# Kernel tuning notes

Measured on AMD Instinct MI355X. Metric: run time of the kernel, lower is better.

Reference implementation:

```python
import jax, jax.numpy as jnp
import numpy as np

B, C, H, W = 8, 256, 64, 64
CQK = C // 8  # 32


def setup_inputs() -> dict:
    key = jax.random.key(0)
    ks = jax.random.split(key, 8)
    s = 0.05
    return {
        "x": jax.random.normal(ks[0], (B, C, H, W), dtype=jnp.float32),
        "wq": jax.random.normal(ks[1], (CQK, C), dtype=jnp.float32) * s,
        "bq": jax.random.normal(ks[2], (CQK,), dtype=jnp.float32) * s,
        "wk": jax.random.normal(ks[3], (CQK, C), dtype=jnp.float32) * s,
        "bk": jax.random.normal(ks[4], (CQK,), dtype=jnp.float32) * s,
        "wv": jax.random.normal(ks[5], (C, C), dtype=jnp.float32) * s,
        "bv": jax.random.normal(ks[6], (C,), dtype=jnp.float32) * s,
        "gamma": jax.random.normal(ks[7], (1,), dtype=jnp.float32),
    }


def reference(x, wq, bq, wk, bk, wv, bv, gamma):
    b, c, h, w = x.shape
    xf = x.reshape(b, c, h * w)  # [B, C, N]
    # conv1d kernel-size-1 == per-token linear over channels
    f = jnp.einsum('oc,bcn->bon', wq, xf) + bq[None, :, None]  # [B, C/8, N]
    g = jnp.einsum('oc,bcn->bon', wk, xf) + bk[None, :, None]  # [B, C/8, N]
    hh = jnp.einsum('oc,bcn->bon', wv, xf) + bv[None, :, None]  # [B, C, N]
    # scores[b, i, j] = sum_o f[b, o, i] * g[b, o, j]; NO 1/sqrt(d) scaling
    scores = jnp.einsum('boi,boj->bij', f, g)  # [B, N, N]
    # softmax over dim=1 (the f/query index axis), as in the original
    beta = jax.nn.softmax(scores, axis=1)
    # o[b, c, j] = gamma * sum_i hh[b, c, i] * beta[b, i, j] + xf
    o = gamma[0] * jnp.einsum('bci,bij->bcj', hh, beta) + xf
    return o.reshape(b, c, h, w)
```

## Files before the change

### kernel.cpp

```cpp
#include <hip/hip_runtime.h>
#include <stdint.h>

#define B_ 8
#define C_ 256
#define N_ 4096
#define LOG2E 1.44269504088896f
#define NSHIFT_L2E (-14.0f * 1.44269504088896f)

typedef _Float16 half8 __attribute__((ext_vector_type(8)));
typedef _Float16 half4 __attribute__((ext_vector_type(4)));
typedef __fp16  fp16x2 __attribute__((ext_vector_type(2)));
typedef float floatx4 __attribute__((ext_vector_type(4)));

__global__ __launch_bounds__(256) void k_wprep(const float* __restrict__ wq, const float* __restrict__ bq,
                                               const float* __restrict__ wk, const float* __restrict__ bk,
                                               const float* __restrict__ wv, const float* __restrict__ bv,
                                               _Float16* __restrict__ Whf, float* __restrict__ Bh) {
    int r = blockIdx.x;
    int t = threadIdx.x;
    const float* src;
    float bias;
    if (r < 32)      { src = wq + r * 256;        bias = bq[r]; }
    else if (r < 64) { src = wk + (r - 32) * 256; bias = bk[r - 32]; }
    else             { src = wv + (r - 64) * 256; bias = bv[r - 64]; }
    Whf[(t >> 3) * 2560 + r * 8 + (t & 7)] = (_Float16)src[t];
    if (t == 0) Bh[r] = bias;
}

__global__ __launch_bounds__(256) void k_proj(const float* __restrict__ x,
                                              const _Float16* __restrict__ Whf,
                                              const float* __restrict__ Bh,
                                              _Float16* __restrict__ Kf,
                                              _Float16* __restrict__ Qf,
                                              _Float16* __restrict__ Vf) {
    __shared__ float xtile[64 * 65];
    __shared__ _Float16 As[64 * 264] __attribute__((aligned(16)));
    int id = blockIdx.x;
    int b  = id & 7;
    int i0 = (id >> 3) * 64;
    int t = threadIdx.x;
    int w = t >> 6, lane = t & 63, col = lane & 15, q = lane >> 4;
    const float* xb = x + (size_t)b * C_ * N_ + i0;
    for (int cc = 0; cc < 4; ++cc) {
        int cr = t >> 4;
        int ip = (t & 15) * 4;
#pragma unroll
        for (int k = 0; k < 4; ++k)
            *(float4*)&xtile[(cr + 16 * k) * 65 + ip] =
                *(const float4*)&xb[(size_t)(cc * 64 + cr + 16 * k) * N_ + ip];
        __syncthreads();
        int i = t & 63, cb2 = (t >> 6) * 16;
        float v[16];
#pragma unroll
        for (int k = 0; k < 16; ++k) v[k] = xtile[(cb2 + k) * 65 + i];
        half8 h0, h1;
#pragma unroll
        for (int k = 0; k < 8; ++k) { h0[k] = (_Float16)v[k]; h1[k] = (_Float16)v[8 + k]; }
        *(half8*)&As[i * 264 + cc * 64 + cb2] = h0;
        *(half8*)&As[i * 264 + cc * 64 + cb2 + 8] = h1;
        __syncthreads();
    }
    floatx4 acc[4][5];
#pragma unroll
    for (int mt = 0; mt < 4; ++mt)
#pragma unroll
        for (int nt = 0; nt < 5; ++nt) acc[mt][nt] = (floatx4){0.f, 0.f, 0.f, 0.f};
    for (int kc = 0; kc < 8; ++kc) {
        half8 a[4], bf[5];
#pragma unroll
        for (int nt = 0; nt < 5; ++nt)
            bf[nt] = *(const half8*)&Whf[(kc * 4 + q) * 2560 + (w * 80 + nt * 16 + col) * 8];
#pragma unroll
        for (int mt = 0; mt < 4; ++mt)
            a[mt] = *(const half8*)&As[(mt * 16 + col) * 264 + kc * 32 + q * 8];
#pragma unroll
        for (int mt = 0; mt < 4; ++mt)
#pragma unroll
            for (int nt = 0; nt < 5; ++nt)
                acc[mt][nt] = __builtin_amdgcn_mfma_f32_16x16x32_f16(a[mt], bf[nt], acc[mt][nt], 0, 0, 0);
    }
#pragma unroll
    for (int nt = 0; nt < 5; ++nt) {
        int n = w * 80 + nt * 16 + col;
        float bias = Bh[n];
        if (n < 32) {
#pragma unroll
            for (int mt = 0; mt < 4; ++mt)
#pragma unroll
                for (int r = 0; r < 4; ++r) {
                    int i = i0 + mt * 16 + q * 4 + r;
                    Kf[((((size_t)b * 128 + (i >> 5)) * 4 + (n >> 3)) * 32 + (i & 31)) * 8 + (n & 7)]
                        = (_Float16)((acc[mt][nt][r] + bias) * LOG2E);
                }
        } else if (n < 64) {
            int n2 = n - 32;
#pragma unroll
            for (int mt = 0; mt < 4; ++mt)
#pragma unroll
                for (int r = 0; r < 4; ++r) {
                    int j = i0 + mt * 16 + q * 4 + r;
                    Qf[((((size_t)b * 128 + (j >> 5)) * 4 + (n2 >> 3)) * 32 + (j & 31)) * 8 + (n2 & 7)]
                        = (_Float16)(acc[mt][nt][r] + bias);
                }
        } else {
            int c = n - 64;
#pragma unroll
            for (int mt = 0; mt < 4; ++mt) {
                int ib = (i0 >> 4) + mt;
                half4 v4;
#pragma unroll
                for (int r = 0; r < 4; ++r) v4[r] = (_Float16)(acc[mt][nt][r] + bias);
                *(half4*)&Vf[(((size_t)b * 256 + ib) * 256 + c) * 16 + q * 4] = v4;
            }
        }
    }
}

#define PS_BUF 4096

#define ATTN_STEP(IT, VCUR, VNXT, ROFF, WOFF)                                     \
    {                                                                             \
        if ((IT) < 63) {                                                          \
            _Pragma("unroll")                                                     \
            for (int ct = 0; ct < 2; ++ct) {                                      \
                VNXT[ct * 2 + 0] = *(const half8*)(pV0 + ct * 256);               \
                VNXT[ct * 2 + 1] = *(const half8*)(pV1 + ct * 256);               \
            }                                                                     \
            pV0 += 16384; pV1 += 16384;                                           \
            aKn0 = *(const half8*)(pK);                                           \
            aKn1 = *(const half8*)(pK + 128);                                     \
            pK += 2048;                                                           \
        }                                                                         \
        _Pragma("unroll")                                                         \
        for (int kk = 0; kk < 2; ++kk) {                                          \
            half8 bfr[4];                                                         \
            _Pragma("unroll")                                                     \
            for (int jt = 0; jt < 4; ++jt)                                        \
                bfr[jt] = *(const half8*)&PsF[(ROFF) + jt * 1024 + (kk ? ro1 : ro0)]; \
            _Pragma("unroll")                                                     \
            for (int ct = 0; ct < 2; ++ct)                                        \
                _Pragma("unroll")                                                 \
                for (int jt = 0; jt < 4; ++jt)                                    \
                    acc[ct][jt] = __builtin_amdgcn_mfma_f32_16x16x32_f16(         \
                        VCUR[ct * 2 + kk], bfr[jt], acc[ct][jt], 0, 0, 0);        \
        }                                                                         \
        if ((IT) < 63) {                                                          \
            _Pragma("unroll")                                                     \
            for (int itl = 0; itl < 2; ++itl) {                                   \
                floatx4 s = __builtin_amdgcn_mfma_f32_16x16x32_f16(               \
                    itl ? aKn1 : aKn0, bq, cns, 0, 0, 0);                         \
                float p0 = exp2f(s[0]);                                           \
                float p1 = exp2f(s[1]);                                           \
                float p2 = exp2f(s[2]);                                           \
                float p3 = exp2f(s[3]);                                           \
                lacc += (p0 + p1) + (p2 + p3);                                    \
                union { fp16x2 v; uint32_t u; } plo, phi;                         \
                plo.v = __builtin_amdgcn_cvt_pkrtz(p0, p1);                       \
                phi.v = __builtin_amdgcn_cvt_pkrtz(p2, p3);                       \
                uint2 pw; pw.x = plo.u; pw.y = phi.u;                             \
                *(uint2*)&PsF[(WOFF) + (itl ? wo1 : wo0)] = pw;                   \
            }                                                                     \
        }                                                                         \
        asm volatile("s_waitcnt lgkmcnt(0)\n\ts_barrier" ::: "memory");           \
    }

__global__ __launch_bounds__(512, 4) void k_attn(const _Float16* __restrict__ Kf,
                                                 const _Float16* __restrict__ Qf,
                                                 const _Float16* __restrict__ Vf,
                                                 const float* __restrict__ x,
                                                 const float* __restrict__ gptr,
                                                 float* __restrict__ out) {
    __shared__ _Float16 PsF[2 * PS_BUF] __attribute__((aligned(16)));
    __shared__ float Lp[2][64];
    int id = blockIdx.x;
    int b  = id & 7;
    int j0 = (id >> 3) * 64;
    int t = threadIdx.x;
    int w = t >> 6, lane = t & 63, col = lane & 15, q = lane >> 4;
    int jts = w & 3, ihs = w >> 2;
    int cw  = w * 32;
    const _Float16* Kfb = Kf + (size_t)b * 131072;
    const _Float16* Qfb = Qf + (size_t)b * 131072;
    const _Float16* Vfb = Vf + (size_t)b * 1048576;
    const _Float16* pK  = Kfb + ((ihs * 4 + q) * 32 + col) * 8;
    const _Float16* pV0 = Vfb + ((q >> 1) * 256 + cw + col) * 16 + (q & 1) * 8;
    const _Float16* pV1 = pV0 + 8192;
    const int cswz = col & 7;
    const int ro0 = col * 64 + ((q ^ cswz) << 3);
    const int ro1 = ro0 ^ 32;
    const int wo0 = (jts * 16 + col) * 64 + (((ihs << 2) ^ (q >> 1) ^ cswz) << 3) + (q & 1) * 4;
    const int wo1 = wo0 ^ 16;
    const floatx4 cns = {NSHIFT_L2E, NSHIFT_L2E, NSHIFT_L2E, NSHIFT_L2E};
    floatx4 acc[2][4];
#pragma unroll
    for (int ct = 0; ct < 2; ++ct)
#pragma unroll
        for (int jt = 0; jt < 4; ++jt) acc[ct][jt] = (floatx4){0.f, 0.f, 0.f, 0.f};
    float lacc = 0.f;
    half8 vA[4], vB[4], aKn0, aKn1;
#pragma unroll
    for (int ct = 0; ct < 2; ++ct) {
        vA[ct * 2 + 0] = *(const half8*)(pV0 + ct * 256);
        vA[ct * 2 + 1] = *(const half8*)(pV1 + ct * 256);
    }
    pV0 += 16384; pV1 += 16384;
    aKn0 = *(const half8*)(pK);
    aKn1 = *(const half8*)(pK + 128);
    pK += 2048;
    int jj = j0 + jts * 16;
    half8 bq = *(const half8*)&Qfb[(((jj >> 5) * 4 + q) * 32 + ((jj & 31) + col)) * 8];
#pragma unroll
    for (int itl = 0; itl < 2; ++itl) {
        floatx4 s = __builtin_amdgcn_mfma_f32_16x16x32_f16(itl ? aKn1 : aKn0, bq, cns, 0, 0, 0);
        float p0 = exp2f(s[0]);
        float p1 = exp2f(s[1]);
        float p2 = exp2f(s[2]);
        float p3 = exp2f(s[3]);
        lacc += (p0 + p1) + (p2 + p3);
        union { fp16x2 v; uint32_t u; } plo, phi;
        plo.v = __builtin_amdgcn_cvt_pkrtz(p0, p1);
        phi.v = __builtin_amdgcn_cvt_pkrtz(p2, p3);
        uint2 pw; pw.x = plo.u; pw.y = phi.u;
        *(uint2*)&PsF[itl ? wo1 : wo0] = pw;
    }
    asm volatile("s_waitcnt lgkmcnt(0)\n\ts_barrier" ::: "memory");
    for (int m = 0; m < 32; ++m) {
        int it = m * 2;
        ATTN_STEP(it,     vA, vB, 0,      PS_BUF)
        ATTN_STEP(it + 1, vB, vA, PS_BUF, 0)
    }
    lacc += __shfl_xor(lacc, 16, 64);
    lacc += __shfl_xor(lacc, 32, 64);
    if (lane < 16) Lp[ihs][jts * 16 + lane] = lacc;
    __syncthreads();
    float gamma = gptr[0];
    const float* xb = x + (size_t)b * C_ * N_;
    float* ob = out + (size_t)b * C_ * N_;
#pragma unroll
    for (int jt = 0; jt < 4; ++jt) {
        int jl = jt * 16 + col;
        float li = 1.0f / (Lp[0][jl] + Lp[1][jl]);
        int j = j0 + jl;
#pragma unroll
        for (int ct = 0; ct < 2; ++ct)
#pragma unroll
            for (int r = 0; r < 4; ++r) {
                int c = cw + ct * 16 + q * 4 + r;
                size_t off = (size_t)c * N_ + j;
                ob[off] = gamma * acc[ct][jt][r] * li + xb[off];
            }
    }
}

extern "C" void kernel_launch(void* const* d_in, const int* in_sizes, int n_in,
                              void* d_out, int out_size, void* d_ws, size_t ws_size,
                              hipStream_t stream) {
    const float* x  = (const float*)d_in[0];
    const float* wq = (const float*)d_in[1];
    const float* bq = (const float*)d_in[2];
    const float* wk = (const float*)d_in[3];
    const float* bk = (const float*)d_in[4];
    const float* wv = (const float*)d_in[5];
    const float* bv = (const float*)d_in[6];
    const float* gm = (const float*)d_in[7];
    float* out = (float*)d_out;
    char* ws = (char*)d_ws;
    _Float16* Vf  = (_Float16*)ws;
    _Float16* Kf  = (_Float16*)(ws + 16777216);
    _Float16* Qf  = (_Float16*)(ws + 18874368);
    _Float16* Whf = (_Float16*)(ws + 20971520);
    float*    Bh  = (float*)(ws + 21135360);

    k_wprep<<<dim3(320), 256, 0, stream>>>(wq, bq, wk, bk, wv, bv, Whf, Bh);
    k_proj<<<dim3(512), 256, 0, stream>>>(x, Whf, Bh, Kf, Qf, Vf);
    k_attn<<<dim3(512), 512, 0, stream>>>(Kf, Qf, Vf, x, gm, out);
}
```

Measured before the change: 190.2 us.

## Enlarge attention tile to 128 query columns per block, halving block count

Each attention block now covers 128 output columns instead of 64, so each V tile loaded from global memory serves twice as many columns and total V traffic is halved. Each wave now owns 64 channels and 64 columns (a 4x4 accumulator tile) and computes all four key sub-blocks for its own 16 columns, which removes the cross-wave partial row-sum combine. The shared P buffer doubles, and register use per thread rises (more accumulators and V fragments), so occupancy drops to 2 blocks per CU and the grid is 256 blocks.

```diff
diff --git a/kernel.cpp b/kernel.cpp
--- a/kernel.cpp
+++ b/kernel.cpp
@@ -116,19 +116,36 @@
     }
 }
 
-#define PS_BUF 4096
+#define PS_HALF 8192
+
+#define ATTN_SBLK(T, AK, WOFF)                                                    \
+    {                                                                             \
+        floatx4 s = __builtin_amdgcn_mfma_f32_16x16x32_f16(AK, bq, cns, 0, 0, 0); \
+        float p0 = exp2f(s[0]);                                                   \
+        float p1 = exp2f(s[1]);                                                   \
+        float p2 = exp2f(s[2]);                                                   \
+        float p3 = exp2f(s[3]);                                                   \
+        lacc += (p0 + p1) + (p2 + p3);                                            \
+        union { fp16x2 v; uint32_t u; } plo, phi;                                 \
+        plo.v = __builtin_amdgcn_cvt_pkrtz(p0, p1);                               \
+        phi.v = __builtin_amdgcn_cvt_pkrtz(p2, p3);                               \
+        uint2 pw; pw.x = plo.u; pw.y = phi.u;                                     \
+        *(uint2*)&PsF[(WOFF) + wo##T] = pw;                                       \
+    }
 
 #define ATTN_STEP(IT, VCUR, VNXT, ROFF, WOFF)                                     \
     {                                                                             \
         if ((IT) < 63) {                                                          \
             _Pragma("unroll")                                                     \
-            for (int ct = 0; ct < 2; ++ct) {                                      \
+            for (int ct = 0; ct < 4; ++ct) {                                      \
                 VNXT[ct * 2 + 0] = *(const half8*)(pV0 + ct * 256);               \
                 VNXT[ct * 2 + 1] = *(const half8*)(pV1 + ct * 256);               \
             }                                                                     \
             pV0 += 16384; pV1 += 16384;                                           \
-            aKn0 = *(const half8*)(pK);                                           \
-            aKn1 = *(const half8*)(pK + 128);                                     \
+            aK0 = *(const half8*)(pK);                                            \
+            aK1 = *(const half8*)(pK + 128);                                      \
+            aK2 = *(const half8*)(pK + 1024);                                     \
+            aK3 = *(const half8*)(pK + 1152);                                     \
             pK += 2048;                                                           \
         }                                                                         \
         _Pragma("unroll")                                                         \
@@ -138,114 +155,96 @@
             for (int jt = 0; jt < 4; ++jt)                                        \
                 bfr[jt] = *(const half8*)&PsF[(ROFF) + jt * 1024 + (kk ? ro1 : ro0)]; \
             _Pragma("unroll")                                                     \
-            for (int ct = 0; ct < 2; ++ct)                                        \
+            for (int ct = 0; ct < 4; ++ct)                                        \
                 _Pragma("unroll")                                                 \
                 for (int jt = 0; jt < 4; ++jt)                                    \
                     acc[ct][jt] = __builtin_amdgcn_mfma_f32_16x16x32_f16(         \
                         VCUR[ct * 2 + kk], bfr[jt], acc[ct][jt], 0, 0, 0);        \
         }                                                                         \
         if ((IT) < 63) {                                                          \
-            _Pragma("unroll")                                                     \
-            for (int itl = 0; itl < 2; ++itl) {                                   \
-                floatx4 s = __builtin_amdgcn_mfma_f32_16x16x32_f16(               \
-                    itl ? aKn1 : aKn0, bq, cns, 0, 0, 0);                         \
-                float p0 = exp2f(s[0]);                                           \
-                float p1 = exp2f(s[1]);                                           \
-                float p2 = exp2f(s[2]);                                           \
-                float p3 = exp2f(s[3]);                                           \
-                lacc += (p0 + p1) + (p2 + p3);                                    \
-                union { fp16x2 v; uint32_t u; } plo, phi;                         \
-                plo.v = __builtin_amdgcn_cvt_pkrtz(p0, p1);                       \
-                phi.v = __builtin_amdgcn_cvt_pkrtz(p2, p3);                       \
-                uint2 pw; pw.x = plo.u; pw.y = phi.u;                             \
-                *(uint2*)&PsF[(WOFF) + (itl ? wo1 : wo0)] = pw;                   \
-            }                                                                     \
+            ATTN_SBLK(0, aK0, WOFF)                                               \
+            ATTN_SBLK(1, aK1, WOFF)                                               \
+            ATTN_SBLK(2, aK2, WOFF)                                               \
+            ATTN_SBLK(3, aK3, WOFF)                                               \
         }                                                                         \
         asm volatile("s_waitcnt lgkmcnt(0)\n\ts_barrier" ::: "memory");           \
     }
 
-__global__ __launch_bounds__(512, 4) void k_attn(const _Float16* __restrict__ Kf,
+__global__ __launch_bounds__(512, 2) void k_attn(const _Float16* __restrict__ Kf,
                                                  const _Float16* __restrict__ Qf,
                                                  const _Float16* __restrict__ Vf,
                                                  const float* __restrict__ x,
                                                  const float* __restrict__ gptr,
                                                  float* __restrict__ out) {
-    __shared__ _Float16 PsF[2 * PS_BUF] __attribute__((aligned(16)));
-    __shared__ float Lp[2][64];
+    __shared__ _Float16 PsF[2 * PS_HALF] __attribute__((aligned(16)));
+    __shared__ float Lp[128];
     int id = blockIdx.x;
     int b  = id & 7;
-    int j0 = (id >> 3) * 64;
+    int j0 = (id >> 3) * 128;
     int t = threadIdx.x;
     int w = t >> 6, lane = t & 63, col = lane & 15, q = lane >> 4;
-    int jts = w & 3, ihs = w >> 2;
-    int cw  = w * 32;
+    int cs = w & 3, jh = w >> 2;
     const _Float16* Kfb = Kf + (size_t)b * 131072;
     const _Float16* Qfb = Qf + (size_t)b * 131072;
     const _Float16* Vfb = Vf + (size_t)b * 1048576;
-    const _Float16* pK  = Kfb + ((ihs * 4 + q) * 32 + col) * 8;
-    const _Float16* pV0 = Vfb + ((q >> 1) * 256 + cw + col) * 16 + (q & 1) * 8;
+    const _Float16* pK  = Kfb + q * 256 + col * 8;
+    const _Float16* pV0 = Vfb + ((q >> 1) * 256 + cs * 64 + col) * 16 + (q & 1) * 8;
     const _Float16* pV1 = pV0 + 8192;
     const int cswz = col & 7;
-    const int ro0 = col * 64 + ((q ^ cswz) << 3);
+    const int ro0 = (jh * 64 + col) * 64 + ((q ^ cswz) << 3);
     const int ro1 = ro0 ^ 32;
-    const int wo0 = (jts * 16 + col) * 64 + (((ihs << 2) ^ (q >> 1) ^ cswz) << 3) + (q & 1) * 4;
-    const int wo1 = wo0 ^ 16;
+    const int wo0 = (w * 16 + col) * 64 + (((0 + (q >> 1)) ^ cswz) << 3) + (q & 1) * 4;
+    const int wo1 = (w * 16 + col) * 64 + (((2 + (q >> 1)) ^ cswz) << 3) + (q & 1) * 4;
+    const int wo2 = (w * 16 + col) * 64 + (((4 + (q >> 1)) ^ cswz) << 3) + (q & 1) * 4;
+    const int wo3 = (w * 16 + col) * 64 + (((6 + (q >> 1)) ^ cswz) << 3) + (q & 1) * 4;
     const floatx4 cns = {NSHIFT_L2E, NSHIFT_L2E, NSHIFT_L2E, NSHIFT_L2E};
-    floatx4 acc[2][4];
-#pragma unroll
-    for (int ct = 0; ct < 2; ++ct)
+    floatx4 acc[4][4];
+#pragma unroll
+    for (int ct = 0; ct < 4; ++ct)
 #pragma unroll
         for (int jt = 0; jt < 4; ++jt) acc[ct][jt] = (floatx4){0.f, 0.f, 0.f, 0.f};
     float lacc = 0.f;
-    half8 vA[4], vB[4], aKn0, aKn1;
-#pragma unroll
-    for (int ct = 0; ct < 2; ++ct) {
+    half8 vA[8], vB[8], aK0, aK1, aK2, aK3;
+#pragma unroll
+    for (int ct = 0; ct < 4; ++ct) {
         vA[ct * 2 + 0] = *(const half8*)(pV0 + ct * 256);
         vA[ct * 2 + 1] = *(const half8*)(pV1 + ct * 256);
     }
     pV0 += 16384; pV1 += 16384;
-    aKn0 = *(const half8*)(pK);
-    aKn1 = *(const half8*)(pK + 128);
+    aK0 = *(const half8*)(pK);
+    aK1 = *(const half8*)(pK + 128);
+    aK2 = *(const half8*)(pK + 1024);
+    aK3 = *(const half8*)(pK + 1152);
     pK += 2048;
-    int jj = j0 + jts * 16;
-    half8 bq = *(const half8*)&Qfb[(((jj >> 5) * 4 + q) * 32 + ((jj & 31) + col)) * 8];
-#pragma unroll
-    for (int itl = 0; itl < 2; ++itl) {
-        floatx4 s = __builtin_amdgcn_mfma_f32_16x16x32_f16(itl ? aKn1 : aKn0, bq, cns, 0, 0, 0);
-        float p0 = exp2f(s[0]);
-        float p1 = exp2f(s[1]);
-        float p2 = exp2f(s[2]);
-        float p3 = exp2f(s[3]);
-        lacc += (p0 + p1) + (p2 + p3);
-        union { fp16x2 v; uint32_t u; } plo, phi;
-        plo.v = __builtin_amdgcn_cvt_pkrtz(p0, p1);
-        phi.v = __builtin_amdgcn_cvt_pkrtz(p2, p3);
-        uint2 pw; pw.x = plo.u; pw.y = phi.u;
-        *(uint2*)&PsF[itl ? wo1 : wo0] = pw;
-    }
+    int jj = j0 + w * 16;
+    half8 bq = *(const half8*)&Qfb[(((jj >> 5) * 4 + q) * 256 + ((jj & 31) + col) * 8)];
+    ATTN_SBLK(0, aK0, 0)
+    ATTN_SBLK(1, aK1, 0)
+    ATTN_SBLK(2, aK2, 0)
+    ATTN_SBLK(3, aK3, 0)
     asm volatile("s_waitcnt lgkmcnt(0)\n\ts_barrier" ::: "memory");
     for (int m = 0; m < 32; ++m) {
         int it = m * 2;
-        ATTN_STEP(it,     vA, vB, 0,      PS_BUF)
-        ATTN_STEP(it + 1, vB, vA, PS_BUF, 0)
+        ATTN_STEP(it,     vA, vB, 0,       PS_HALF)
+        ATTN_STEP(it + 1, vB, vA, PS_HALF, 0)
     }
     lacc += __shfl_xor(lacc, 16, 64);
     lacc += __shfl_xor(lacc, 32, 64);
-    if (lane < 16) Lp[ihs][jts * 16 + lane] = lacc;
+    if (lane < 16) Lp[w * 16 + lane] = lacc;
     __syncthreads();
     float gamma = gptr[0];
     const float* xb = x + (size_t)b * C_ * N_;
     float* ob = out + (size_t)b * C_ * N_;
 #pragma unroll
     for (int jt = 0; jt < 4; ++jt) {
-        int jl = jt * 16 + col;
-        float li = 1.0f / (Lp[0][jl] + Lp[1][jl]);
+        int jl = jh * 64 + jt * 16 + col;
+        float li = 1.0f / Lp[jl];
         int j = j0 + jl;
 #pragma unroll
-        for (int ct = 0; ct < 2; ++ct)
+        for (int ct = 0; ct < 4; ++ct)
 #pragma unroll
             for (int r = 0; r < 4; ++r) {
-                int c = cw + ct * 16 + q * 4 + r;
+                int c = cs * 64 + ct * 16 + q * 4 + r;
                 size_t off = (size_t)c * N_ + j;
                 ob[off] = gamma * acc[ct][jt][r] * li + xb[off];
             }
@@ -273,5 +272,5 @@
 
     k_wprep<<<dim3(320), 256, 0, stream>>>(wq, bq, wk, bk, wv, bv, Whf, Bh);
     k_proj<<<dim3(512), 256, 0, stream>>>(x, Whf, Bh, Kf, Qf, Vf);
-    k_attn<<<dim3(512), 512, 0, stream>>>(Kf, Qf, Vf, x, gm, out);
-}
+    k_attn<<<dim3(256), 512, 0, stream>>>(Kf, Qf, Vf, x, gm, out);
+}
```

Result: slower. 208.4 us (+9.6%).

## Double the i-block per barrier and raise MFMA wave priority

Applied to the files above, without the earlier changes.

Each barrier-separated step of the attention loop now covers two 64-row i-blocks: the P staging buffer doubles to 8192 halves per buffer, the loop runs 16 iterations of paired steps instead of 32, and the shared-memory swizzle offsets are rewritten for the wider row stride. This halves the number of workgroup barriers and lets score computation for two sub-blocks interleave with the PV MFMAs. s_setprio is raised around the PV MFMA block so waves issuing matrix work get scheduling priority. The cost is more LDS per block (32 KB vs 16 KB), which may lower occupancy at 4 blocks per CU, and more complex indexing.

```diff
diff --git a/kernel.cpp b/kernel.cpp
--- a/kernel.cpp
+++ b/kernel.cpp
@@ -116,51 +116,65 @@
     }
 }
 
-#define PS_BUF 4096
-
-#define ATTN_STEP(IT, VCUR, VNXT, ROFF, WOFF)                                     \
+#define PS_BUF 8192
+
+#define ATTN_SBLK(AK, WO)                                                         \
     {                                                                             \
-        if ((IT) < 63) {                                                          \
+        floatx4 s = __builtin_amdgcn_mfma_f32_16x16x32_f16(AK, bq, cns, 0, 0, 0); \
+        float p0 = exp2f(s[0]);                                                   \
+        float p1 = exp2f(s[1]);                                                   \
+        float p2 = exp2f(s[2]);                                                   \
+        float p3 = exp2f(s[3]);                                                   \
+        lacc += (p0 + p1) + (p2 + p3);                                            \
+        union { fp16x2 v; uint32_t u; } plo, phi;                                 \
+        plo.v = __builtin_amdgcn_cvt_pkrtz(p0, p1);                               \
+        phi.v = __builtin_amdgcn_cvt_pkrtz(p2, p3);                               \
+        uint2 pw; pw.x = plo.u; pw.y = phi.u;                                     \
+        *(uint2*)&PsF[WO] = pw;                                                   \
+    }
+
+#define ATTN_SUB(COND, H, VC, VN, KKA, KKB, ROFF, WOFF)                           \
+    {                                                                             \
+        if (COND) {                                                               \
+            aK0 = *(const half8*)(pK);                                            \
+            aK1 = *(const half8*)(pK + 128);                                      \
+            pK += 2048;                                                           \
+        }                                                                         \
+        if ((H) == 0 || (COND)) {                                                 \
             _Pragma("unroll")                                                     \
             for (int ct = 0; ct < 2; ++ct) {                                      \
-                VNXT[ct * 2 + 0] = *(const half8*)(pV0 + ct * 256);               \
-                VNXT[ct * 2 + 1] = *(const half8*)(pV1 + ct * 256);               \
+                VN[ct * 2 + 0] = *(const half8*)(pV0 + ct * 256);                 \
+                VN[ct * 2 + 1] = *(const half8*)(pV1 + ct * 256);                 \
             }                                                                     \
             pV0 += 16384; pV1 += 16384;                                           \
-            aKn0 = *(const half8*)(pK);                                           \
-            aKn1 = *(const half8*)(pK + 128);                                     \
-            pK += 2048;                                                           \
-        }                                                                         \
+        }                                                                         \
+        __builtin_amdgcn_s_setprio(1);                                            \
         _Pragma("unroll")                                                         \
         for (int kk = 0; kk < 2; ++kk) {                                          \
             half8 bfr[4];                                                         \
             _Pragma("unroll")                                                     \
             for (int jt = 0; jt < 4; ++jt)                                        \
-                bfr[jt] = *(const half8*)&PsF[(ROFF) + jt * 1024 + (kk ? ro1 : ro0)]; \
+                bfr[jt] = *(const half8*)&PsF[(ROFF) + jt * 2048 +                \
+                    ((kk ? (KKB) : (KKA)) & 1 ? ro1 : ro0) +                      \
+                    ((kk ? (KKB) : (KKA)) >> 1) * 64];                            \
             _Pragma("unroll")                                                     \
             for (int ct = 0; ct < 2; ++ct)                                        \
                 _Pragma("unroll")                                                 \
                 for (int jt = 0; jt < 4; ++jt)                                    \
                     acc[ct][jt] = __builtin_amdgcn_mfma_f32_16x16x32_f16(         \
-                        VCUR[ct * 2 + kk], bfr[jt], acc[ct][jt], 0, 0, 0);        \
-        }                                                                         \
-        if ((IT) < 63) {                                                          \
-            _Pragma("unroll")                                                     \
-            for (int itl = 0; itl < 2; ++itl) {                                   \
-                floatx4 s = __builtin_amdgcn_mfma_f32_16x16x32_f16(               \
-                    itl ? aKn1 : aKn0, bq, cns, 0, 0, 0);                         \
-                float p0 = exp2f(s[0]);                                           \
-                float p1 = exp2f(s[1]);                                           \
-                float p2 = exp2f(s[2]);                                           \
-                float p3 = exp2f(s[3]);                                           \
-                lacc += (p0 + p1) + (p2 + p3);                                    \
-                union { fp16x2 v; uint32_t u; } plo, phi;                         \
-                plo.v = __builtin_amdgcn_cvt_pkrtz(p0, p1);                       \
-                phi.v = __builtin_amdgcn_cvt_pkrtz(p2, p3);                       \
-                uint2 pw; pw.x = plo.u; pw.y = phi.u;                             \
-                *(uint2*)&PsF[(WOFF) + (itl ? wo1 : wo0)] = pw;                   \
-            }                                                                     \
-        }                                                                         \
+                        VC[ct * 2 + kk], bfr[jt], acc[ct][jt], 0, 0, 0);          \
+        }                                                                         \
+        __builtin_amdgcn_s_setprio(0);                                            \
+        if (COND) {                                                               \
+            ATTN_SBLK(aK0, (WOFF) + wo0 + (H) * 64)                               \
+            ATTN_SBLK(aK1, (WOFF) + wo1 + (H) * 64)                               \
+        }                                                                         \
+    }
+
+#define ATTN_STEP(IT, ROFF, WOFF)                                                 \
+    {                                                                             \
+        ATTN_SUB((IT) < 31, 0, vA, vB, 0, 1, ROFF, WOFF)                          \
+        ATTN_SUB((IT) < 31, 1, vB, vA, 2, 3, ROFF, WOFF)                          \
         asm volatile("s_waitcnt lgkmcnt(0)\n\ts_barrier" ::: "memory");           \
     }
 
@@ -186,9 +200,9 @@
     const _Float16* pV0 = Vfb + ((q >> 1) * 256 + cw + col) * 16 + (q & 1) * 8;
     const _Float16* pV1 = pV0 + 8192;
     const int cswz = col & 7;
-    const int ro0 = col * 64 + ((q ^ cswz) << 3);
+    const int ro0 = col * 128 + ((q ^ cswz) << 3);
     const int ro1 = ro0 ^ 32;
-    const int wo0 = (jts * 16 + col) * 64 + (((ihs << 2) ^ (q >> 1) ^ cswz) << 3) + (q & 1) * 4;
+    const int wo0 = (jts * 16 + col) * 128 + ((((ihs << 2) + (q >> 1)) ^ cswz) << 3) + (q & 1) * 4;
     const int wo1 = wo0 ^ 16;
     const floatx4 cns = {NSHIFT_L2E, NSHIFT_L2E, NSHIFT_L2E, NSHIFT_L2E};
     floatx4 acc[2][4];
@@ -197,37 +211,28 @@
 #pragma unroll
         for (int jt = 0; jt < 4; ++jt) acc[ct][jt] = (floatx4){0.f, 0.f, 0.f, 0.f};
     float lacc = 0.f;
-    half8 vA[4], vB[4], aKn0, aKn1;
+    half8 vA[4], vB[4], aK0, aK1;
 #pragma unroll
     for (int ct = 0; ct < 2; ++ct) {
         vA[ct * 2 + 0] = *(const half8*)(pV0 + ct * 256);
         vA[ct * 2 + 1] = *(const half8*)(pV1 + ct * 256);
     }
     pV0 += 16384; pV1 += 16384;
-    aKn0 = *(const half8*)(pK);
-    aKn1 = *(const half8*)(pK + 128);
-    pK += 2048;
     int jj = j0 + jts * 16;
     half8 bq = *(const half8*)&Qfb[(((jj >> 5) * 4 + q) * 32 + ((jj & 31) + col)) * 8];
 #pragma unroll
-    for (int itl = 0; itl < 2; ++itl) {
-        floatx4 s = __builtin_amdgcn_mfma_f32_16x16x32_f16(itl ? aKn1 : aKn0, bq, cns, 0, 0, 0);
-        float p0 = exp2f(s[0]);
-        float p1 = exp2f(s[1]);
-        float p2 = exp2f(s[2]);
-        float p3 = exp2f(s[3]);
-        lacc += (p0 + p1) + (p2 + p3);
-        union { fp16x2 v; uint32_t u; } plo, phi;
-        plo.v = __builtin_amdgcn_cvt_pkrtz(p0, p1);
-        phi.v = __builtin_amdgcn_cvt_pkrtz(p2, p3);
-        uint2 pw; pw.x = plo.u; pw.y = phi.u;
-        *(uint2*)&PsF[itl ? wo1 : wo0] = pw;
+    for (int h = 0; h < 2; ++h) {
+        aK0 = *(const half8*)(pK);
+        aK1 = *(const half8*)(pK + 128);
+        pK += 2048;
+        ATTN_SBLK(aK0, wo0 + h * 64)
+        ATTN_SBLK(aK1, wo1 + h * 64)
     }
     asm volatile("s_waitcnt lgkmcnt(0)\n\ts_barrier" ::: "memory");
-    for (int m = 0; m < 32; ++m) {
+    for (int m = 0; m < 16; ++m) {
         int it = m * 2;
-        ATTN_STEP(it,     vA, vB, 0,      PS_BUF)
-        ATTN_STEP(it + 1, vB, vA, PS_BUF, 0)
+        ATTN_STEP(it,     0,      PS_BUF)
+        ATTN_STEP(it + 1, PS_BUF, 0)
     }
     lacc += __shfl_xor(lacc, 16, 64);
     lacc += __shfl_xor(lacc, 32, 64);
```

After: 190.9 us. No clear change (+0.4%).
